# Kernel tuning notes

Hardware: AMD Instinct MI355X
Metric: run time of the kernel (lower is better)

## Reference

```python
import jax, jax.numpy as jnp
import numpy as np

HIDDEN = 1024
SEQ = 32768


def setup_inputs() -> dict:
    key = jax.random.key(0)
    k1, k2, k3, k4 = jax.random.split(key, 4)
    scale = 1.0 / np.sqrt(HIDDEN)
    return {
        "hidden": jax.random.normal(k1, (HIDDEN,), dtype=jnp.float32),
        "encoder_outputs": jax.random.normal(k2, (SEQ, HIDDEN), dtype=jnp.float32),
        "W": jax.random.normal(k3, (HIDDEN, HIDDEN), dtype=jnp.float32) * scale,
        "b": jax.random.normal(k4, (HIDDEN,), dtype=jnp.float32) * scale,
    }


def reference(hidden, encoder_outputs, W, b):
    # method == 'general': energy_i = Linear(enc_i); score_i = hidden . energy_i
    # Batched: energies = (enc @ W.T + b) @ hidden   -> [S]
    proj = jnp.einsum("sh,oh->so", encoder_outputs, W) + b  # [S, H]
    energies = proj @ hidden                                  # [S]
    attn = jax.nn.softmax(energies, axis=-1)                  # softmax over seq
    return attn[None, None, :]                                # [1, 1, S]
```

## Files before the change

kernel.cpp:

```cpp
#include <hip/hip_runtime.h>
#include <math.h>

#define H 1024
#define S 32768

typedef float f32x4 __attribute__((ext_vector_type(4)));

__global__ void matvec_v_kernel(const float* __restrict__ W,
                                const float* __restrict__ hidden,
                                float* __restrict__ v) {
    __shared__ float sh[H];
    __shared__ float4 red[256];
    const int t = threadIdx.x;
    const int b = blockIdx.x;
    const int c = t & 3;
    const int j = t >> 2;

    *reinterpret_cast<float4*>(&sh[t * 4]) =
        *reinterpret_cast<const float4*>(&hidden[t * 4]);
    __syncthreads();

    const int colbase = b * 16 + c * 4;
    float4 acc = make_float4(0.f, 0.f, 0.f, 0.f);
#pragma unroll
    for (int k = 0; k < 16; ++k) {
        const int o = j + 64 * k;
        const float hv = sh[o];
        const f32x4 w = __builtin_nontemporal_load(
            reinterpret_cast<const f32x4*>(&W[(size_t)o * H + colbase]));
        acc.x += hv * w.x; acc.y += hv * w.y;
        acc.z += hv * w.z; acc.w += hv * w.w;
    }
    red[t] = acc;
    __syncthreads();
#pragma unroll
    for (int off = 128; off >= 4; off >>= 1) {
        if (t < off) {
            float4 a = red[t], bb = red[t + off];
            a.x += bb.x; a.y += bb.y; a.z += bb.z; a.w += bb.w;
            red[t] = a;
        }
        __syncthreads();
    }
    if (t < 4)
        *reinterpret_cast<float4*>(&v[b * 16 + t * 4]) = red[t];
}

__global__ void energies_kernel(const float* __restrict__ enc,
                                const float* __restrict__ v,
                                float* __restrict__ energies,
                                float* __restrict__ mpart,
                                float* __restrict__ spart) {
    __shared__ float sv[H];
    __shared__ float lm[4], ls[4];
    const int t = threadIdx.x;
    const int wave = t >> 6;
    const int lane = t & 63;
    const int grp  = lane >> 4;
    const int gl   = lane & 15;

    *reinterpret_cast<float4*>(&sv[t * 4]) =
        *reinterpret_cast<const float4*>(&v[t * 4]);

    const int row = blockIdx.x * 16 + wave * 4 + grp;
    const f32x4* rp = reinterpret_cast<const f32x4*>(
        enc + (size_t)row * H + gl * 4);
    __syncthreads();

    f32x4 ev[8];
    float acc = 0.f;

#pragma unroll
    for (int s = 0; s < 8; ++s)
        ev[s] = __builtin_nontemporal_load(rp + s * 16);
#pragma unroll
    for (int s = 0; s < 8; ++s) {
        const float4 vv = *reinterpret_cast<const float4*>(&sv[s * 64 + gl * 4]);
        acc += ev[s].x * vv.x + ev[s].y * vv.y + ev[s].z * vv.z + ev[s].w * vv.w;
    }
#pragma unroll
    for (int s = 0; s < 8; ++s)
        ev[s] = __builtin_nontemporal_load(rp + (s + 8) * 16);
#pragma unroll
    for (int s = 0; s < 8; ++s) {
        const float4 vv = *reinterpret_cast<const float4*>(&sv[(s + 8) * 64 + gl * 4]);
        acc += ev[s].x * vv.x + ev[s].y * vv.y + ev[s].z * vv.z + ev[s].w * vv.w;
    }

#pragma unroll
    for (int off = 1; off <= 8; off <<= 1)
        acc += __shfl_xor(acc, off, 64);

    float mw = acc;
    mw = fmaxf(mw, __shfl_xor(mw, 16, 64));
    mw = fmaxf(mw, __shfl_xor(mw, 32, 64));
    float sw = __expf(acc - mw);
    sw += __shfl_xor(sw, 16, 64);
    sw += __shfl_xor(sw, 32, 64);

    if (gl == 0) energies[row] = acc;
    if (lane == 0) { lm[wave] = mw; ls[wave] = sw; }
    __syncthreads();
    if (t == 0) {
        const float m = fmaxf(fmaxf(lm[0], lm[1]), fmaxf(lm[2], lm[3]));
        const float s = ls[0] * __expf(lm[0] - m) + ls[1] * __expf(lm[1] - m) +
                        ls[2] * __expf(lm[2] - m) + ls[3] * __expf(lm[3] - m);
        mpart[blockIdx.x] = m;
        spart[blockIdx.x] = s;
    }
}

__global__ void finalize_kernel(const float* __restrict__ energies,
                                const float* __restrict__ mpart,
                                const float* __restrict__ spart,
                                float* __restrict__ out) {
    const int t = threadIdx.x;
    const int lane = t & 63;
    const int wave = t >> 6;
    __shared__ float rm[4], rs[4];

    const float4 ma = *reinterpret_cast<const float4*>(&mpart[t * 8]);
    const float4 mb = *reinterpret_cast<const float4*>(&mpart[t * 8 + 4]);
    const float4 sa = *reinterpret_cast<const float4*>(&spart[t * 8]);
    const float4 sb = *reinterpret_cast<const float4*>(&spart[t * 8 + 4]);

    float mt = fmaxf(fmaxf(fmaxf(ma.x, ma.y), fmaxf(ma.z, ma.w)),
                     fmaxf(fmaxf(mb.x, mb.y), fmaxf(mb.z, mb.w)));
#pragma unroll
    for (int off = 32; off > 0; off >>= 1)
        mt = fmaxf(mt, __shfl_xor(mt, off, 64));
    if (lane == 0) rm[wave] = mt;
    __syncthreads();
    const float gm = fmaxf(fmaxf(rm[0], rm[1]), fmaxf(rm[2], rm[3]));

    float st = sa.x * __expf(ma.x - gm) + sa.y * __expf(ma.y - gm) +
               sa.z * __expf(ma.z - gm) + sa.w * __expf(ma.w - gm) +
               sb.x * __expf(mb.x - gm) + sb.y * __expf(mb.y - gm) +
               sb.z * __expf(mb.z - gm) + sb.w * __expf(mb.w - gm);
#pragma unroll
    for (int off = 32; off > 0; off >>= 1)
        st += __shfl_xor(st, off, 64);
    if (lane == 0) rs[wave] = st;
    __syncthreads();
    const float inv = 1.0f / (rs[0] + rs[1] + rs[2] + rs[3]);

    const int i = blockIdx.x * 256 + t;
    out[i] = __expf(energies[i] - gm) * inv;
}

extern "C" void kernel_launch(void* const* d_in, const int* in_sizes, int n_in,
                              void* d_out, int out_size, void* d_ws, size_t ws_size,
                              hipStream_t stream) {
    const float* hidden = (const float*)d_in[0];
    const float* enc    = (const float*)d_in[1];
    const float* W      = (const float*)d_in[2];
    float* out = (float*)d_out;

    float* v        = (float*)d_ws;
    float* energies = v + H;
    float* mpart    = energies + S;
    float* spart    = mpart + 2048;

    matvec_v_kernel<<<64, 256, 0, stream>>>(W, hidden, v);
    energies_kernel<<<2048, 256, 0, stream>>>(enc, v, energies, mpart, spart);
    finalize_kernel<<<128, 256, 0, stream>>>(energies, mpart, spart, out);
}
```

Baseline: 199.4 us.

## Fuse energies and softmax finalize via cooperative launch with atomic grid barrier

Merges the energies and finalize kernels into one cooperatively launched kernel. Blocks publish their partial max and sum, then spin on an atomic counter until every block has arrived. After that, each block reduces all partials and writes its normalized outputs straight from registers. This drops one kernel launch and the write and reread of the energies array, at the cost of a grid-wide spin barrier that requires all 2048 blocks to be resident; if the cooperative launch fails, it falls back to the original two kernels.

Result: slower. 499.7 us (+150.6%).

```diff
diff --git a/kernel.cpp b/kernel.cpp
--- a/kernel.cpp
+++ b/kernel.cpp
@@ -1,18 +1,23 @@
 #include <hip/hip_runtime.h>
+#include <hip/hip_cooperative_groups.h>
 #include <math.h>
 
 #define H 1024
 #define S 32768
+#define GRID2 2048
+#define TPB 256
 
 typedef float f32x4 __attribute__((ext_vector_type(4)));
 
 __global__ void matvec_v_kernel(const float* __restrict__ W,
                                 const float* __restrict__ hidden,
-                                float* __restrict__ v) {
+                                float* __restrict__ v,
+                                unsigned int* __restrict__ done) {
     __shared__ float sh[H];
     __shared__ float4 red[256];
     const int t = threadIdx.x;
     const int b = blockIdx.x;
+    if (b == 0 && t == 0) *done = 0u;
     const int c = t & 3;
     const int j = t >> 2;
 
@@ -46,6 +51,112 @@
         *reinterpret_cast<float4*>(&v[b * 16 + t * 4]) = red[t];
 }
 
+extern "C" __global__ void __launch_bounds__(TPB, 8)
+energies_finalize_kernel(const float* __restrict__ enc,
+                         const float* __restrict__ v,
+                         float* __restrict__ mpart,
+                         float* __restrict__ spart,
+                         unsigned int* __restrict__ done,
+                         float* __restrict__ out) {
+    __shared__ float sv[H];
+    __shared__ float lm[4], ls[4];
+    __shared__ float rm[4], rs[4];
+    const int t = threadIdx.x;
+    const int wave = t >> 6;
+    const int lane = t & 63;
+    const int grp  = lane >> 4;
+    const int gl   = lane & 15;
+
+    *reinterpret_cast<float4*>(&sv[t * 4]) =
+        *reinterpret_cast<const float4*>(&v[t * 4]);
+
+    const int row = blockIdx.x * 16 + wave * 4 + grp;
+    const f32x4* rp = reinterpret_cast<const f32x4*>(
+        enc + (size_t)row * H + gl * 4);
+    __syncthreads();
+
+    f32x4 ev[8];
+    float acc = 0.f;
+#pragma unroll
+    for (int s = 0; s < 8; ++s)
+        ev[s] = __builtin_nontemporal_load(rp + s * 16);
+#pragma unroll
+    for (int s = 0; s < 8; ++s) {
+        const float4 vv = *reinterpret_cast<const float4*>(&sv[s * 64 + gl * 4]);
+        acc += ev[s].x * vv.x + ev[s].y * vv.y + ev[s].z * vv.z + ev[s].w * vv.w;
+    }
+#pragma unroll
+    for (int s = 0; s < 8; ++s)
+        ev[s] = __builtin_nontemporal_load(rp + (s + 8) * 16);
+#pragma unroll
+    for (int s = 0; s < 8; ++s) {
+        const float4 vv = *reinterpret_cast<const float4*>(&sv[(s + 8) * 64 + gl * 4]);
+        acc += ev[s].x * vv.x + ev[s].y * vv.y + ev[s].z * vv.z + ev[s].w * vv.w;
+    }
+
+#pragma unroll
+    for (int off = 1; off <= 8; off <<= 1)
+        acc += __shfl_xor(acc, off, 64);
+
+    float mw = acc;
+    mw = fmaxf(mw, __shfl_xor(mw, 16, 64));
+    mw = fmaxf(mw, __shfl_xor(mw, 32, 64));
+    float sw = __expf(acc - mw);
+    sw += __shfl_xor(sw, 16, 64);
+    sw += __shfl_xor(sw, 32, 64);
+
+    if (lane == 0) { lm[wave] = mw; ls[wave] = sw; }
+    __syncthreads();
+
+    if (t == 0) {
+        const float m = fmaxf(fmaxf(lm[0], lm[1]), fmaxf(lm[2], lm[3]));
+        const float s = ls[0] * __expf(lm[0] - m) + ls[1] * __expf(lm[1] - m) +
+                        ls[2] * __expf(lm[2] - m) + ls[3] * __expf(lm[3] - m);
+        __hip_atomic_store(&mpart[blockIdx.x], m, __ATOMIC_RELAXED,
+                           __HIP_MEMORY_SCOPE_AGENT);
+        __hip_atomic_store(&spart[blockIdx.x], s, __ATOMIC_RELAXED,
+                           __HIP_MEMORY_SCOPE_AGENT);
+        __hip_atomic_fetch_add(done, 1u, __ATOMIC_RELEASE,
+                               __HIP_MEMORY_SCOPE_AGENT);
+        while (__hip_atomic_load(done, __ATOMIC_ACQUIRE,
+                                 __HIP_MEMORY_SCOPE_AGENT) < GRID2)
+            __builtin_amdgcn_s_sleep(8);
+    }
+    __syncthreads();
+
+    float mv[8], s8[8];
+#pragma unroll
+    for (int k = 0; k < 8; ++k)
+        mv[k] = __hip_atomic_load(&mpart[k * 256 + t], __ATOMIC_RELAXED,
+                                  __HIP_MEMORY_SCOPE_AGENT);
+#pragma unroll
+    for (int k = 0; k < 8; ++k)
+        s8[k] = __hip_atomic_load(&spart[k * 256 + t], __ATOMIC_RELAXED,
+                                  __HIP_MEMORY_SCOPE_AGENT);
+
+    float mt = mv[0];
+#pragma unroll
+    for (int k = 1; k < 8; ++k) mt = fmaxf(mt, mv[k]);
+#pragma unroll
+    for (int off = 32; off > 0; off >>= 1)
+        mt = fmaxf(mt, __shfl_xor(mt, off, 64));
+    if (lane == 0) rm[wave] = mt;
+    __syncthreads();
+    const float gm = fmaxf(fmaxf(rm[0], rm[1]), fmaxf(rm[2], rm[3]));
+
+    float st = 0.f;
+#pragma unroll
+    for (int k = 0; k < 8; ++k) st += s8[k] * __expf(mv[k] - gm);
+#pragma unroll
+    for (int off = 32; off > 0; off >>= 1)
+        st += __shfl_xor(st, off, 64);
+    if (lane == 0) rs[wave] = st;
+    __syncthreads();
+    const float inv = 1.0f / (rs[0] + rs[1] + rs[2] + rs[3]);
+
+    if (gl == 0) out[row] = __expf(acc - gm) * inv;
+}
+
 __global__ void energies_kernel(const float* __restrict__ enc,
                                 const float* __restrict__ v,
                                 float* __restrict__ energies,
@@ -69,7 +180,6 @@
 
     f32x4 ev[8];
     float acc = 0.f;
-
 #pragma unroll
     for (int s = 0; s < 8; ++s)
         ev[s] = __builtin_nontemporal_load(rp + s * 16);
@@ -86,7 +196,6 @@
         const float4 vv = *reinterpret_cast<const float4*>(&sv[(s + 8) * 64 + gl * 4]);
         acc += ev[s].x * vv.x + ev[s].y * vv.y + ev[s].z * vv.z + ev[s].w * vv.w;
     }
-
 #pragma unroll
     for (int off = 1; off <= 8; off <<= 1)
         acc += __shfl_xor(acc, off, 64);
@@ -157,11 +266,21 @@
     float* out = (float*)d_out;
 
     float* v        = (float*)d_ws;
-    float* energies = v + H;
-    float* mpart    = energies + S;
+    float* mpart    = v + H;
     float* spart    = mpart + 2048;
-
-    matvec_v_kernel<<<64, 256, 0, stream>>>(W, hidden, v);
-    energies_kernel<<<2048, 256, 0, stream>>>(enc, v, energies, mpart, spart);
-    finalize_kernel<<<128, 256, 0, stream>>>(energies, mpart, spart, out);
-}
+    unsigned int* done = (unsigned int*)(spart + 2048);
+    float* energies = (float*)(done + 16);
+
+    matvec_v_kernel<<<64, 256, 0, stream>>>(W, hidden, v, done);
+
+    void* args[] = { (void*)&enc, (void*)&v, (void*)&mpart, (void*)&spart,
+                     (void*)&done, (void*)&out };
+    hipError_t err = hipLaunchCooperativeKernel(
+        reinterpret_cast<void*>(energies_finalize_kernel),
+        dim3(GRID2), dim3(TPB), args, 0, stream);
+
+    if (err != hipSuccess) {
+        energies_kernel<<<2048, 256, 0, stream>>>(enc, v, energies, mpart, spart);
+        finalize_kernel<<<128, 256, 0, stream>>>(energies, mpart, spart, out);
+    }
+}
```
